# Kernel tuning notes

Measured on AMD Instinct MI355X. Metric: run time of the kernel, lower is better.

## Reference

```python
import jax, jax.numpy as jnp
import numpy as np

NUM_HEADS = 16
NHID = 64
D = NUM_HEADS * NHID  # 1024, also keys/query/values dim and out_dim
SL, BS = 2048, 32


def setup_inputs() -> dict:
    key = jax.random.key(0)
    ks = jax.random.split(key, 7)
    s = 1.0 / np.sqrt(D)
    return {
        "query": jax.random.normal(ks[0], (BS, D), jnp.float32),
        "keys": jax.random.normal(ks[1], (SL, BS, D), jnp.float32),
        "values": jax.random.normal(ks[2], (SL, BS, D), jnp.float32),
        "Wq": jax.random.normal(ks[3], (D, D), jnp.float32) * s,
        "Wk": jax.random.normal(ks[4], (D, D), jnp.float32) * s,
        "Wv": jax.random.normal(ks[5], (D, D), jnp.float32) * s,
        "Wo": jax.random.normal(ks[6], (D, D), jnp.float32) * s,
    }


def reference(query, keys, values, Wq, Wk, Wv, Wo):
    sl, bs, _ = keys.shape
    qp = query @ Wq.T                       # [bs, H*nhid]
    kp = keys @ Wk.T                        # [sl, bs, H*nhid]
    vp = values @ Wv.T                      # [sl, bs, H*nhid]
    # elementwise multiplicative score, reduced per head
    dot = (qp * kp).reshape(sl, bs, NUM_HEADS, NHID).sum(-1) / np.sqrt(NHID)
    # NOTE: original uses log_softmax (not softmax) over the sequence dim
    w = jax.nn.log_softmax(dot, axis=0)[..., None]        # [sl, bs, H, 1]
    attn = (w * vp.reshape(sl, bs, NUM_HEADS, NHID)).sum(0)  # [bs, H, nhid]
    return attn.reshape(bs, -1) @ Wo.T                     # [bs, D]
```

## Files before the change

kernel.cpp:

```cpp
#include <hip/hip_runtime.h>

#define SL  2048
#define BSZ 32
#define DIM 1024
#define NH  16
#define HD  64

typedef __attribute__((ext_vector_type(4))) float f32x4;
typedef __attribute__((ext_vector_type(8))) short s16x8;

static __device__ __forceinline__ short f2bf(float f) {
    union { float f; unsigned u; } v; v.f = f;
    unsigned r = (v.u + 0x7fffu + ((v.u >> 16) & 1u)) >> 16;
    return (short)r;
}

__global__ __launch_bounds__(128) void k_gemm32(const float* __restrict__ A,
                                                const float* __restrict__ W,
                                                float* __restrict__ O,
                                                int rmul, int hsel) {
    int oc = blockIdx.x & 15;
    int bg = blockIdx.x >> 4;
    int wv = __builtin_amdgcn_readfirstlane(threadIdx.x >> 6);
    int lane = threadIdx.x & 63;
    int b = bg * 2 + wv;
    int o = oc * 64 + lane;
    int row = b * rmul + (hsel ? oc : 0);
    const float* arow = A + (size_t)row * DIM;
    const float* wrow = W + (size_t)o * DIM;
    f32x4 acc = {0.f, 0.f, 0.f, 0.f};
#pragma unroll 4
    for (int k = 0; k < DIM; k += 4) {
        f32x4 a = *(const f32x4*)(arow + k);
        f32x4 w = *(const f32x4*)(wrow + k);
        acc += a * w;
    }
    O[(size_t)b * DIM + o] = acc[0] + acc[1] + acc[2] + acc[3];
}

__global__ __launch_bounds__(256) void k_ut(const float* __restrict__ qp,
                                            const float* __restrict__ Wk,
                                            short* __restrict__ u) {
    int idx = blockIdx.x;
    int jc = idx & 15;
    int h  = (idx >> 4) & 15;
    int bg = idx >> 8;
    int wv = __builtin_amdgcn_readfirstlane(threadIdx.x >> 6);
    int lane = threadIdx.x & 63;
    int b = bg * 4 + wv;
    int j = jc * 64 + lane;
    const float* qrow = qp + (size_t)b * DIM + h * HD;
    const float* wcol = Wk + (size_t)(h * HD) * DIM + j;
    float acc = 0.f;
#pragma unroll 8
    for (int i = 0; i < HD; ++i) acc += qrow[i] * wcol[(size_t)i * DIM];
    u[((size_t)(b * NH + h)) * DIM + j] = f2bf(acc * 0.125f);
}

__global__ __launch_bounds__(256) void k_dot(const float* __restrict__ keys,
                                             const short* __restrict__ u,
                                             float* __restrict__ dot) {
    int b  = blockIdx.x & 31;
    int s0 = (blockIdx.x >> 5) * 128;
    __shared__ short ulds[NH][DIM + 8];
    {
        const uint4* src = (const uint4*)(u + (size_t)b * NH * DIM);
        for (int idx = threadIdx.x; idx < NH * DIM / 8; idx += 256) {
            int row = idx >> 7;
            int col = (idx & 127) * 8;
            *(uint4*)&ulds[row][col] = src[idx];
        }
    }
    __syncthreads();
    int lane = threadIdx.x & 63;
    int wave = threadIdx.x >> 6;
    int lrow = lane & 15;
    int kgrp = lane >> 4;
    f32x4 acc0 = {0.f,0.f,0.f,0.f}, acc1 = {0.f,0.f,0.f,0.f};
    const float* ka = keys + ((size_t)(s0 + wave * 32 + lrow) * BSZ + b) * DIM;
    const float* kb = ka + (size_t)16 * BSZ * DIM;
#pragma unroll 2
    for (int k0 = 0; k0 < DIM; k0 += 32) {
        int kj = k0 + kgrp * 8;
        s16x8 bf = *(const s16x8*)&ulds[lrow][kj];
        f32x4 a0 = *(const f32x4*)(ka + kj);
        f32x4 a1 = *(const f32x4*)(ka + kj + 4);
        s16x8 af;
        af[0]=f2bf(a0[0]); af[1]=f2bf(a0[1]); af[2]=f2bf(a0[2]); af[3]=f2bf(a0[3]);
        af[4]=f2bf(a1[0]); af[5]=f2bf(a1[1]); af[6]=f2bf(a1[2]); af[7]=f2bf(a1[3]);
        acc0 = __builtin_amdgcn_mfma_f32_16x16x32_bf16(af, bf, acc0, 0, 0, 0);
        f32x4 c0 = *(const f32x4*)(kb + kj);
        f32x4 c1 = *(const f32x4*)(kb + kj + 4);
        s16x8 ag;
        ag[0]=f2bf(c0[0]); ag[1]=f2bf(c0[1]); ag[2]=f2bf(c0[2]); ag[3]=f2bf(c0[3]);
        ag[4]=f2bf(c1[0]); ag[5]=f2bf(c1[1]); ag[6]=f2bf(c1[2]); ag[7]=f2bf(c1[3]);
        acc1 = __builtin_amdgcn_mfma_f32_16x16x32_bf16(ag, bf, acc1, 0, 0, 0);
    }
    size_t obase = ((size_t)b * SL + (s0 + wave * 32 + kgrp * 4)) * NH + lrow;
#pragma unroll
    for (int r = 0; r < 4; ++r) {
        dot[obase + (size_t)r * NH]        = acc0[r];
        dot[obase + (size_t)(16 + r) * NH] = acc1[r];
    }
}

__global__ __launch_bounds__(1024) void k_red(const float* __restrict__ dot,
                                              float* __restrict__ T) {
    int b = blockIdx.x, t = threadIdx.x;
    const f32x4* base = (const f32x4*)(dot + (size_t)b * SL * NH);
    __shared__ f32x4 red[1024];
    __shared__ float Mh[16];
    f32x4 m = {-1e30f, -1e30f, -1e30f, -1e30f};
#pragma unroll
    for (int k = 0; k < 8; ++k) {
        f32x4 v = base[t + k * 1024];
        m[0]=fmaxf(m[0],v[0]); m[1]=fmaxf(m[1],v[1]);
        m[2]=fmaxf(m[2],v[2]); m[3]=fmaxf(m[3],v[3]);
    }
    red[t] = m;
    __syncthreads();
    for (int s = 512; s >= 4; s >>= 1) {
        if (t < s) {
            f32x4 a = red[t], c = red[t + s];
            a[0]=fmaxf(a[0],c[0]); a[1]=fmaxf(a[1],c[1]);
            a[2]=fmaxf(a[2],c[2]); a[3]=fmaxf(a[3],c[3]);
            red[t] = a;
        }
        __syncthreads();
    }
    if (t < 4) { f32x4 mm = red[t]; for (int i = 0; i < 4; ++i) Mh[t*4+i] = mm[i]; }
    __syncthreads();
    int hq = t & 3;
    f32x4 M4;
    M4[0]=Mh[hq*4]; M4[1]=Mh[hq*4+1]; M4[2]=Mh[hq*4+2]; M4[3]=Mh[hq*4+3];
    f32x4 ssum = {0.f,0.f,0.f,0.f};
#pragma unroll
    for (int k = 0; k < 8; ++k) {
        f32x4 v = base[t + k * 1024];
        ssum[0]+=__expf(v[0]-M4[0]); ssum[1]+=__expf(v[1]-M4[1]);
        ssum[2]+=__expf(v[2]-M4[2]); ssum[3]+=__expf(v[3]-M4[3]);
    }
    __syncthreads();
    red[t] = ssum;
    __syncthreads();
    for (int s = 512; s >= 4; s >>= 1) {
        if (t < s) {
            f32x4 a = red[t], c = red[t + s];
            a += c;
            red[t] = a;
        }
        __syncthreads();
    }
    if (t < 4) {
        f32x4 ss = red[t];
        for (int i = 0; i < 4; ++i)
            T[b * NH + t * 4 + i] = Mh[t * 4 + i] + __logf(ss[i]);
    }
}

__global__ __launch_bounds__(256) void k_z(const float* __restrict__ values,
                                           const float* __restrict__ w,
                                           const float* __restrict__ T,
                                           float* __restrict__ z) {
    int b  = blockIdx.x & 31;
    int jc = blockIdx.x >> 5;
    int t = threadIdx.x;
    int ssub = t >> 4;
    int jq = t & 15;
    int j = jc * 64 + jq * 4;
    f32x4 acc[NH];
#pragma unroll
    for (int h = 0; h < NH; ++h) acc[h] = (f32x4){0.f,0.f,0.f,0.f};
    f32x4 accV = {0.f,0.f,0.f,0.f};
    const float* vbase = values + (size_t)b * DIM + j;
    const float* wbase = w + (size_t)b * SL * NH;
#pragma unroll 4
    for (int s = ssub; s < SL; s += 16) {
        f32x4 v = *(const f32x4*)(vbase + (size_t)s * (BSZ * DIM));
        const f32x4* wr = (const f32x4*)(wbase + s * NH);
        float ws[16];
        *(f32x4*)(ws + 0)  = wr[0];
        *(f32x4*)(ws + 4)  = wr[1];
        *(f32x4*)(ws + 8)  = wr[2];
        *(f32x4*)(ws + 12) = wr[3];
#pragma unroll
        for (int h = 0; h < NH; ++h) acc[h] += v * ws[h];
        accV += v;
    }
    __shared__ f32x4 lds[16 * 16 * 16];
#pragma unroll
    for (int h = 0; h < NH; ++h) lds[(ssub * 16 + h) * 16 + jq] = acc[h];
    __syncthreads();
    int h2 = t >> 4, q = t & 15;
    f32x4 sumW = {0.f,0.f,0.f,0.f};
#pragma unroll
    for (int sub = 0; sub < 16; ++sub) sumW += lds[(sub * 16 + h2) * 16 + q];
    __syncthreads();
    lds[ssub * 16 + jq] = accV;
    __syncthreads();
    f32x4 sumV = {0.f,0.f,0.f,0.f};
#pragma unroll
    for (int sub = 0; sub < 16; ++sub) sumV += lds[sub * 16 + q];
    float Th = T[b * NH + h2];
    f32x4 zv = sumW - Th * sumV;
    *(f32x4*)(z + ((size_t)(b * NH + h2)) * DIM + jc * 64 + q * 4) = zv;
}

extern "C" void kernel_launch(void* const* d_in, const int* in_sizes, int n_in,
                              void* d_out, int out_size, void* d_ws, size_t ws_size,
                              hipStream_t stream) {
    const float* query  = (const float*)d_in[0];
    const float* keys   = (const float*)d_in[1];
    const float* values = (const float*)d_in[2];
    const float* Wq = (const float*)d_in[3];
    const float* Wk = (const float*)d_in[4];
    const float* Wv = (const float*)d_in[5];
    const float* Wo = (const float*)d_in[6];
    float* out = (float*)d_out;

    char* ws = (char*)d_ws;
    float* qp   = (float*)(ws + 0);
    short* u    = (short*)(ws + (128 << 10));
    float* dotb = (float*)(ws + (128 << 10) + (1 << 20));
    float* z    = (float*)(ws + (128 << 10) + (5 << 20));
    float* attn = (float*)(ws + (128 << 10) + (7 << 20));
    float* T    = (float*)(ws + (256 << 10) + (7 << 20));

    hipLaunchKernelGGL(k_gemm32, dim3(256),  dim3(128), 0, stream, query, Wq, qp, 1, 0);
    hipLaunchKernelGGL(k_ut,     dim3(2048), dim3(256), 0, stream, qp, Wk, u);
    hipLaunchKernelGGL(k_dot,    dim3(512),  dim3(256), 0, stream, keys, u, dotb);
    hipLaunchKernelGGL(k_red,    dim3(32),   dim3(1024),0, stream, dotb, T);
    hipLaunchKernelGGL(k_z,      dim3(512),  dim3(256), 0, stream, values, dotb, T, z);
    hipLaunchKernelGGL(k_gemm32, dim3(256),  dim3(128), 0, stream, z, Wv, attn, 16, 1);
    hipLaunchKernelGGL(k_gemm32, dim3(256),  dim3(128), 0, stream, attn, Wo, out, 1, 0);
}
```

Before: 241.9 us.

## Split K in small GEMMs, halve dot tiles, split value-reduction over sequence

The small GEMMs now split the K dimension across four waves and combine the partials through shared memory. The dot kernel now uses one 16-row MFMA tile per wave, which doubles the grid. The value-weighting kernel splits the sequence into two halves written to separate z buffers, which the Wv GEMM sums while loading its input. It also stages the log-softmax weights in LDS and reduces partials with wave shuffles. The goal is more parallelism for kernels that were starved of blocks and latency-bound, at the cost of extra shared-memory reductions and one more z buffer.

New measurement: 199.1 us. 1.21x faster.

```diff
diff --git a/kernel.cpp b/kernel.cpp
--- a/kernel.cpp
+++ b/kernel.cpp
@@ -15,27 +15,35 @@
     return (short)r;
 }
 
-__global__ __launch_bounds__(128) void k_gemm32(const float* __restrict__ A,
-                                                const float* __restrict__ W,
-                                                float* __restrict__ O,
-                                                int rmul, int hsel) {
+template<bool DUAL>
+__global__ __launch_bounds__(256) void k_gemm(const float* __restrict__ A,
+                                              const float* __restrict__ A2,
+                                              const float* __restrict__ W,
+                                              float* __restrict__ O,
+                                              int rmul, int hsel) {
     int oc = blockIdx.x & 15;
-    int bg = blockIdx.x >> 4;
+    int b  = blockIdx.x >> 4;
     int wv = __builtin_amdgcn_readfirstlane(threadIdx.x >> 6);
     int lane = threadIdx.x & 63;
-    int b = bg * 2 + wv;
     int o = oc * 64 + lane;
     int row = b * rmul + (hsel ? oc : 0);
-    const float* arow = A + (size_t)row * DIM;
-    const float* wrow = W + (size_t)o * DIM;
+    const float* arow  = A + (size_t)row * DIM + wv * 256;
+    const float* a2row = DUAL ? (A2 + (size_t)row * DIM + wv * 256) : nullptr;
+    const float* wrow  = W + (size_t)o * DIM + wv * 256;
     f32x4 acc = {0.f, 0.f, 0.f, 0.f};
 #pragma unroll 4
-    for (int k = 0; k < DIM; k += 4) {
+    for (int k = 0; k < 256; k += 4) {
         f32x4 a = *(const f32x4*)(arow + k);
+        if (DUAL) a += *(const f32x4*)(a2row + k);
         f32x4 w = *(const f32x4*)(wrow + k);
         acc += a * w;
     }
-    O[(size_t)b * DIM + o] = acc[0] + acc[1] + acc[2] + acc[3];
+    __shared__ float red[4][64];
+    red[wv][lane] = acc[0] + acc[1] + acc[2] + acc[3];
+    __syncthreads();
+    int t = threadIdx.x;
+    if (t < 64)
+        O[(size_t)b * DIM + oc * 64 + t] = red[0][t] + red[1][t] + red[2][t] + red[3][t];
 }
 
 __global__ __launch_bounds__(256) void k_ut(const float* __restrict__ qp,
@@ -57,11 +65,11 @@
     u[((size_t)(b * NH + h)) * DIM + j] = f2bf(acc * 0.125f);
 }
 
-__global__ __launch_bounds__(256) void k_dot(const float* __restrict__ keys,
-                                             const short* __restrict__ u,
-                                             float* __restrict__ dot) {
+__global__ __launch_bounds__(256, 4) void k_dot(const float* __restrict__ keys,
+                                                const short* __restrict__ u,
+                                                float* __restrict__ dot) {
     int b  = blockIdx.x & 31;
-    int s0 = (blockIdx.x >> 5) * 128;
+    int s0 = (blockIdx.x >> 5) * 64;
     __shared__ short ulds[NH][DIM + 8];
     {
         const uint4* src = (const uint4*)(u + (size_t)b * NH * DIM);
@@ -76,10 +84,9 @@
     int wave = threadIdx.x >> 6;
     int lrow = lane & 15;
     int kgrp = lane >> 4;
-    f32x4 acc0 = {0.f,0.f,0.f,0.f}, acc1 = {0.f,0.f,0.f,0.f};
-    const float* ka = keys + ((size_t)(s0 + wave * 32 + lrow) * BSZ + b) * DIM;
-    const float* kb = ka + (size_t)16 * BSZ * DIM;
-#pragma unroll 2
+    f32x4 acc = {0.f, 0.f, 0.f, 0.f};
+    const float* ka = keys + ((size_t)(s0 + wave * 16 + lrow) * BSZ + b) * DIM;
+#pragma unroll 4
     for (int k0 = 0; k0 < DIM; k0 += 32) {
         int kj = k0 + kgrp * 8;
         s16x8 bf = *(const s16x8*)&ulds[lrow][kj];
@@ -88,20 +95,12 @@
         s16x8 af;
         af[0]=f2bf(a0[0]); af[1]=f2bf(a0[1]); af[2]=f2bf(a0[2]); af[3]=f2bf(a0[3]);
         af[4]=f2bf(a1[0]); af[5]=f2bf(a1[1]); af[6]=f2bf(a1[2]); af[7]=f2bf(a1[3]);
-        acc0 = __builtin_amdgcn_mfma_f32_16x16x32_bf16(af, bf, acc0, 0, 0, 0);
-        f32x4 c0 = *(const f32x4*)(kb + kj);
-        f32x4 c1 = *(const f32x4*)(kb + kj + 4);
-        s16x8 ag;
-        ag[0]=f2bf(c0[0]); ag[1]=f2bf(c0[1]); ag[2]=f2bf(c0[2]); ag[3]=f2bf(c0[3]);
-        ag[4]=f2bf(c1[0]); ag[5]=f2bf(c1[1]); ag[6]=f2bf(c1[2]); ag[7]=f2bf(c1[3]);
-        acc1 = __builtin_amdgcn_mfma_f32_16x16x32_bf16(ag, bf, acc1, 0, 0, 0);
-    }
-    size_t obase = ((size_t)b * SL + (s0 + wave * 32 + kgrp * 4)) * NH + lrow;
-#pragma unroll
-    for (int r = 0; r < 4; ++r) {
-        dot[obase + (size_t)r * NH]        = acc0[r];
-        dot[obase + (size_t)(16 + r) * NH] = acc1[r];
-    }
+        acc = __builtin_amdgcn_mfma_f32_16x16x32_bf16(af, bf, acc, 0, 0, 0);
+    }
+    size_t obase = ((size_t)b * SL + (s0 + wave * 16 + kgrp * 4)) * NH + lrow;
+#pragma unroll
+    for (int r = 0; r < 4; ++r)
+        dot[obase + (size_t)r * NH] = acc[r];
 }
 
 __global__ __launch_bounds__(1024) void k_red(const float* __restrict__ dot,
@@ -144,11 +143,7 @@
     red[t] = ssum;
     __syncthreads();
     for (int s = 512; s >= 4; s >>= 1) {
-        if (t < s) {
-            f32x4 a = red[t], c = red[t + s];
-            a += c;
-            red[t] = a;
-        }
+        if (t < s) { f32x4 a = red[t]; a += red[t + s]; red[t] = a; }
         __syncthreads();
     }
     if (t < 4) {
@@ -158,52 +153,87 @@
     }
 }
 
-__global__ __launch_bounds__(256) void k_z(const float* __restrict__ values,
-                                           const float* __restrict__ w,
-                                           const float* __restrict__ T,
-                                           float* __restrict__ z) {
-    int b  = blockIdx.x & 31;
-    int jc = blockIdx.x >> 5;
-    int t = threadIdx.x;
+__global__ __launch_bounds__(256, 4) void k_z(const float* __restrict__ values,
+                                              const float* __restrict__ w,
+                                              const float* __restrict__ T,
+                                              float* __restrict__ z) {
+    int x  = blockIdx.x;
+    int b  = x & 31;
+    int jc = (x >> 5) & 15;
+    int sh = x >> 9;
+    int t  = threadIdx.x;
     int ssub = t >> 4;
     int jq = t & 15;
     int j = jc * 64 + jq * 4;
+    int wv = __builtin_amdgcn_readfirstlane(t >> 6);
+    int lane = t & 63;
+
+    __shared__ float wlds[128 * 16];
+    __shared__ f32x4 redW[4][16][16];
+    __shared__ f32x4 redV[4][16];
+
     f32x4 acc[NH];
 #pragma unroll
     for (int h = 0; h < NH; ++h) acc[h] = (f32x4){0.f,0.f,0.f,0.f};
     f32x4 accV = {0.f,0.f,0.f,0.f};
+
     const float* vbase = values + (size_t)b * DIM + j;
-    const float* wbase = w + (size_t)b * SL * NH;
+    const float* wbase = w + ((size_t)b * SL + sh * 1024) * NH;
+
+    for (int ph = 0; ph < 8; ++ph) {
+        if (ph) __syncthreads();
+        {
+            const f32x4* src = (const f32x4*)(wbase + ph * 128 * NH);
+            f32x4* dst = (f32x4*)wlds;
+            dst[t]       = src[t];
+            dst[t + 256] = src[t + 256];
+        }
+        __syncthreads();
+        int sbase = sh * 1024 + ph * 128;
 #pragma unroll 4
-    for (int s = ssub; s < SL; s += 16) {
-        f32x4 v = *(const f32x4*)(vbase + (size_t)s * (BSZ * DIM));
-        const f32x4* wr = (const f32x4*)(wbase + s * NH);
-        float ws[16];
-        *(f32x4*)(ws + 0)  = wr[0];
-        *(f32x4*)(ws + 4)  = wr[1];
-        *(f32x4*)(ws + 8)  = wr[2];
-        *(f32x4*)(ws + 12) = wr[3];
-#pragma unroll
-        for (int h = 0; h < NH; ++h) acc[h] += v * ws[h];
-        accV += v;
-    }
-    __shared__ f32x4 lds[16 * 16 * 16];
-#pragma unroll
-    for (int h = 0; h < NH; ++h) lds[(ssub * 16 + h) * 16 + jq] = acc[h];
+        for (int it = 0; it < 8; ++it) {
+            int s_loc = it * 16 + ssub;
+            f32x4 v = *(const f32x4*)(vbase + (size_t)(sbase + s_loc) * (BSZ * DIM));
+            const float* wr = wlds + s_loc * 16;
+#pragma unroll
+            for (int h = 0; h < NH; ++h) {
+                float wh = wr[h];
+                acc[h] += v * wh;
+            }
+            accV += v;
+        }
+    }
+
+#pragma unroll
+    for (int h = 0; h < NH; ++h) {
+#pragma unroll
+        for (int e = 0; e < 4; ++e) {
+            float x0 = acc[h][e];
+            x0 += __shfl_xor(x0, 16);
+            x0 += __shfl_xor(x0, 32);
+            acc[h][e] = x0;
+        }
+    }
+#pragma unroll
+    for (int e = 0; e < 4; ++e) {
+        float x0 = accV[e];
+        x0 += __shfl_xor(x0, 16);
+        x0 += __shfl_xor(x0, 32);
+        accV[e] = x0;
+    }
+    if (lane < 16) {
+#pragma unroll
+        for (int h = 0; h < NH; ++h) redW[wv][h][lane] = acc[h];
+        redV[wv][lane] = accV;
+    }
     __syncthreads();
     int h2 = t >> 4, q = t & 15;
-    f32x4 sumW = {0.f,0.f,0.f,0.f};
-#pragma unroll
-    for (int sub = 0; sub < 16; ++sub) sumW += lds[(sub * 16 + h2) * 16 + q];
-    __syncthreads();
-    lds[ssub * 16 + jq] = accV;
-    __syncthreads();
-    f32x4 sumV = {0.f,0.f,0.f,0.f};
-#pragma unroll
-    for (int sub = 0; sub < 16; ++sub) sumV += lds[sub * 16 + q];
+    f32x4 sumW = redW[0][h2][q] + redW[1][h2][q] + redW[2][h2][q] + redW[3][h2][q];
+    f32x4 sumV = redV[0][q] + redV[1][q] + redV[2][q] + redV[3][q];
     float Th = T[b * NH + h2];
     f32x4 zv = sumW - Th * sumV;
-    *(f32x4*)(z + ((size_t)(b * NH + h2)) * DIM + jc * 64 + q * 4) = zv;
+    float* zp = z + (size_t)sh * (BSZ * NH * DIM);
+    *(f32x4*)(zp + ((size_t)(b * NH + h2)) * DIM + jc * 64 + q * 4) = zv;
 }
 
 extern "C" void kernel_launch(void* const* d_in, const int* in_sizes, int n_in,
@@ -222,15 +252,16 @@
     float* qp   = (float*)(ws + 0);
     short* u    = (short*)(ws + (128 << 10));
     float* dotb = (float*)(ws + (128 << 10) + (1 << 20));
-    float* z    = (float*)(ws + (128 << 10) + (5 << 20));
-    float* attn = (float*)(ws + (128 << 10) + (7 << 20));
-    float* T    = (float*)(ws + (256 << 10) + (7 << 20));
-
-    hipLaunchKernelGGL(k_gemm32, dim3(256),  dim3(128), 0, stream, query, Wq, qp, 1, 0);
-    hipLaunchKernelGGL(k_ut,     dim3(2048), dim3(256), 0, stream, qp, Wk, u);
-    hipLaunchKernelGGL(k_dot,    dim3(512),  dim3(256), 0, stream, keys, u, dotb);
-    hipLaunchKernelGGL(k_red,    dim3(32),   dim3(1024),0, stream, dotb, T);
-    hipLaunchKernelGGL(k_z,      dim3(512),  dim3(256), 0, stream, values, dotb, T, z);
-    hipLaunchKernelGGL(k_gemm32, dim3(256),  dim3(128), 0, stream, z, Wv, attn, 16, 1);
-    hipLaunchKernelGGL(k_gemm32, dim3(256),  dim3(128), 0, stream, attn, Wo, out, 1, 0);
-}
+    float* z0   = (float*)(ws + (128 << 10) + (5 << 20));
+    float* z1   = (float*)(ws + (128 << 10) + (7 << 20));
+    float* attn = (float*)(ws + (128 << 10) + (9 << 20));
+    float* T    = (float*)(ws + (256 << 10) + (9 << 20));
+
+    hipLaunchKernelGGL(k_gemm<false>, dim3(512),  dim3(256), 0, stream, query, nullptr, Wq, qp, 1, 0);
+    hipLaunchKernelGGL(k_ut,          dim3(2048), dim3(256), 0, stream, qp, Wk, u);
+    hipLaunchKernelGGL(k_dot,         dim3(1024), dim3(256), 0, stream, keys, u, dotb);
+    hipLaunchKernelGGL(k_red,         dim3(32),   dim3(1024),0, stream, dotb, T);
+    hipLaunchKernelGGL(k_z,           dim3(1024), dim3(256), 0, stream, values, dotb, T, z0);
+    hipLaunchKernelGGL(k_gemm<true>,  dim3(512),  dim3(256), 0, stream, z0, z1, Wv, attn, 16, 1);
+    hipLaunchKernelGGL(k_gemm<false>, dim3(512),  dim3(256), 0, stream, attn, nullptr, Wo, out, 1, 0);
+}
```
